# Kernel optimization log

Measured on AMD Instinct MI355X. Metric: run time of the kernel, lower is better.

Reference implementation:

```python
import jax, jax.numpy as jnp
import numpy as np

NUM_HEADS = 8

def setup_inputs() -> dict:
    key = jax.random.key(0)
    ks = jax.random.split(key, 7)
    B, N, K, C = 4, 16384, 16, 64
    pcd = jax.random.normal(ks[0], (B, C, N), dtype=jnp.float32)
    neighbors = jax.random.normal(ks[1], (B, C, N, K), dtype=jnp.float32)
    xyz = jax.random.normal(ks[2], (B, 3, N), dtype=jnp.float32)
    idx_all = jax.random.randint(ks[3], (B, N, K), 0, N)
    Wq = jax.random.normal(ks[4], (C, C + 3), dtype=jnp.float32) * 0.1
    Wk = jax.random.normal(ks[5], (C, C + 3), dtype=jnp.float32) * 0.1
    Wv = jax.random.normal(ks[6], (C, C + 3), dtype=jnp.float32) * 0.1
    return {"pcd": pcd, "neighbors": neighbors, "xyz": xyz,
            "Wq": Wq, "Wk": Wk, "Wv": Wv, "idx_all": idx_all}


def reference(pcd, neighbors, xyz, Wq, Wk, Wv, idx_all):
    B, C, N = pcd.shape
    K = neighbors.shape[-1]
    H = NUM_HEADS
    D = C // H
    # --- query: concat xyz, 1x1 conv, split heads ---
    pcd_cat = jnp.concatenate([pcd, xyz], axis=1)                 # (B, C+3, N)
    q = jnp.einsum('oc,bcn->bon', Wq, pcd_cat)                    # (B, C, N)
    q = q.reshape(B, H, D, N).transpose(0, 1, 3, 2)               # (B, H, N, D)
    # --- index_points: gather xyz at KNN indices (irregular gather) ---
    xyz_t = xyz.transpose(0, 2, 1)                                # (B, N, 3)
    rel_xyz = jax.vmap(lambda pts, ix: pts[ix])(xyz_t, idx_all)   # (B, N, K, 3)
    nb = jnp.concatenate([neighbors, rel_xyz.transpose(0, 3, 1, 2)], axis=1)  # (B, C+3, N, K)
    # --- key/value: 1x1 conv + split heads ---
    k = jnp.einsum('oc,bcnk->bonk', Wk, nb).reshape(B, H, D, N, K).transpose(0, 1, 3, 4, 2)  # (B,H,N,K,D)
    v = jnp.einsum('oc,bcnk->bonk', Wv, nb).reshape(B, H, D, N, K).transpose(0, 1, 3, 4, 2)  # (B,H,N,K,D)
    # --- local scalar-dot attention over the K neighbors of each point ---
    energy = jnp.einsum('bhnd,bhnkd->bhnk', q, k) / jnp.sqrt(jnp.float32(D))  # (B,H,N,K)
    attn = jax.nn.softmax(energy, axis=-1)
    x = jnp.einsum('bhnk,bhnkd->bhnd', attn, v)                   # (B, H, N, D)
    # (B,H,N,D) -> (B,N,H*D) -> (B, C, N), matching torch reshape/permute order
    out = x.transpose(0, 2, 1, 3).reshape(B, N, H * D).transpose(0, 2, 1)
    return out
```

## Files before the change

kernel.cpp:

```cpp
#include <hip/hip_runtime.h>
#include <math.h>

#define B_ 4
#define C_ 64
#define N_ 16384
#define K_ 16
#define H_ 8
#define CP 67
#define CPAD 68
#define NP 16
#define QSTRIDE 65
#define ESTRIDE 552

__device__ __align__(16) float wpad[3 * C_ * CPAD];

__global__ void setup_weights(const float* __restrict__ Wq,
                              const float* __restrict__ Wk,
                              const float* __restrict__ Wv) {
  int i = blockIdx.x * blockDim.x + threadIdx.x;
  if (i >= C_ * CPAD) return;
  int o = i / CPAD, j = i - o * CPAD;
  float q = 0.f, kk = 0.f, v = 0.f;
  if (j < CP) {
    q = Wq[o * CP + j] * 0.35355339059327373f;
    kk = Wk[o * CP + j];
    v = Wv[o * CP + j];
  }
  wpad[i] = q;
  wpad[C_ * CPAD + i] = kk;
  wpad[2 * C_ * CPAD + i] = v;
}

#define SWZ(v, imm) __int_as_float(__builtin_amdgcn_ds_swizzle(__float_as_int(v), (imm)))
#define XOR1 0x041F
#define XOR2 0x081F
#define XOR4 0x101F
#define XOR8 0x201F

__launch_bounds__(256, 3)
__global__ void pt_attn(const float* __restrict__ pcd,
                        const float* __restrict__ neighbors,
                        const float* __restrict__ xyz,
                        const int* __restrict__ idx_all,
                        float* __restrict__ out) {
  __shared__ __align__(16) float x_lds[NP * CPAD];
  __shared__ float q_lds[NP * QSTRIDE];
  __shared__ __align__(16) float e_lds[NP * ESTRIDE];

  const int tid = threadIdx.x;
  const int p = tid >> 4;
  const int k = tid & 15;
  const int blk = blockIdx.x;
  const int b = blk >> 10;
  const int n0 = (blk & 1023) << 4;
  const int n = n0 + p;

  float nb[CPAD];
  {
    const float* gp = neighbors + (size_t)b * (C_ * N_ * K_) + n0 * K_ + tid;
#pragma unroll
    for (int c = 0; c < C_; ++c)
      nb[c] = gp[(size_t)c * (N_ * K_)];
  }
  {
    const int idx = idx_all[(b * N_ + n) * K_ + k];
    const float* gx = xyz + (size_t)b * (3 * N_) + idx;
    nb[64] = gx[0];
    nb[65] = gx[N_];
    nb[66] = gx[2 * N_];
    nb[67] = 0.f;
  }

  {
    const int pp = tid & 15;
    const int c0 = tid >> 4;
#pragma unroll
    for (int it = 0; it < 4; ++it) {
      int c = c0 + it * 16;
      x_lds[pp * CPAD + c] = pcd[((size_t)b * C_ + c) * N_ + n0 + pp];
    }
    if (tid < 48)
      x_lds[pp * CPAD + 64 + c0] = xyz[((size_t)b * 3 + c0) * N_ + n0 + pp];
    if (tid < 16)
      x_lds[pp * CPAD + 67] = 0.f;
  }
  __syncthreads();

  {
    const float4* xr = (const float4*)(x_lds + p * CPAD);
    const float4* wq = (const float4*)(wpad) + 4 * k * 17;
    float a0 = 0.f, a1 = 0.f, a2 = 0.f, a3 = 0.f;
#pragma unroll
    for (int j4 = 0; j4 < 17; ++j4) {
      float4 xv = xr[j4];
      float4 w0 = wq[j4];
      float4 w1 = wq[17 + j4];
      float4 w2 = wq[34 + j4];
      float4 w3 = wq[51 + j4];
      a0 += w0.x * xv.x + w0.y * xv.y + w0.z * xv.z + w0.w * xv.w;
      a1 += w1.x * xv.x + w1.y * xv.y + w1.z * xv.z + w1.w * xv.w;
      a2 += w2.x * xv.x + w2.y * xv.y + w2.z * xv.z + w2.w * xv.w;
      a3 += w3.x * xv.x + w3.y * xv.y + w3.z * xv.z + w3.w * xv.w;
    }
    q_lds[p * QSTRIDE + 4 * k + 0] = a0;
    q_lds[p * QSTRIDE + 4 * k + 1] = a1;
    q_lds[p * QSTRIDE + 4 * k + 2] = a2;
    q_lds[p * QSTRIDE + 4 * k + 3] = a3;
  }
  __syncthreads();

  {
    const int h = k & 7;
    const int jh = k >> 3;
    float qa[8];
#pragma unroll
    for (int d = 0; d < 8; ++d)
      qa[d] = q_lds[p * QSTRIDE + h * 8 + d];
    const float4* wk = (const float4*)(wpad + C_ * CPAD) + h * 8 * 17;
    float4* er = (float4*)(e_lds + p * ESTRIDE + h * CPAD);
#pragma unroll
    for (int u = 0; u < 9; ++u) {
      int j4 = jh * 8 + u;
      float4 a = make_float4(0.f, 0.f, 0.f, 0.f);
#pragma unroll
      for (int d = 0; d < 8; ++d) {
        float4 w = wk[d * 17 + j4];
        a.x += qa[d] * w.x;
        a.y += qa[d] * w.y;
        a.z += qa[d] * w.z;
        a.w += qa[d] * w.w;
      }
      er[j4] = a;
    }
  }
  __syncthreads();

  float en[8];
#pragma unroll
  for (int h = 0; h < 8; ++h) en[h] = 0.f;
  {
    const float4* ep = (const float4*)(e_lds + p * ESTRIDE);
#pragma unroll
    for (int j4 = 0; j4 < 17; ++j4) {
#pragma unroll
      for (int h = 0; h < 8; ++h) {
        float4 e4 = ep[h * 17 + j4];
        en[h] += e4.x * nb[4 * j4 + 0] + e4.y * nb[4 * j4 + 1] +
                 e4.z * nb[4 * j4 + 2] + e4.w * nb[4 * j4 + 3];
      }
    }
  }
  float at[8];
#pragma unroll
  for (int h = 0; h < 8; ++h) {
    float m = en[h];
    m = fmaxf(m, SWZ(m, XOR1));
    m = fmaxf(m, SWZ(m, XOR2));
    m = fmaxf(m, SWZ(m, XOR4));
    m = fmaxf(m, SWZ(m, XOR8));
    float e = __expf(en[h] - m);
    float s = e;
    s += SWZ(s, XOR1);
    s += SWZ(s, XOR2);
    s += SWZ(s, XOR4);
    s += SWZ(s, XOR8);
    at[h] = e * __builtin_amdgcn_rcpf(s);
  }

  float ap[8];
  {
    const bool g2 = (k & 8) != 0;
    const bool g1 = (k & 4) != 0;
    const bool g0 = (k & 2) != 0;
    float t0[8], t1[8];
#pragma unroll
    for (int i = 0; i < 8; ++i) t0[i] = g2 ? at[i ^ 4] : at[i];
#pragma unroll
    for (int i = 0; i < 8; ++i) t1[i] = g1 ? t0[i ^ 2] : t0[i];
#pragma unroll
    for (int i = 0; i < 8; ++i) ap[i] = g0 ? t1[i ^ 1] : t1[i];
  }

  float xo0 = 0.f, xo1 = 0.f, xo2 = 0.f, xo3 = 0.f;
  const float4* wv = (const float4*)(wpad + 2 * C_ * CPAD) + 4 * k * 17;
#pragma unroll
  for (int j4 = 0; j4 < 17; ++j4) {
    float agg0, agg1, agg2, agg3;
#pragma unroll
    for (int u = 0; u < 4; ++u) {
      float nbj = nb[4 * j4 + u];
      float s0 = ap[0] * nbj, s1 = ap[1] * nbj, s2 = ap[2] * nbj, s3 = ap[3] * nbj;
      float s4 = ap[4] * nbj, s5 = ap[5] * nbj, s6 = ap[6] * nbj, s7 = ap[7] * nbj;
      s0 += SWZ(s4, XOR8);
      s1 += SWZ(s5, XOR8);
      s2 += SWZ(s6, XOR8);
      s3 += SWZ(s7, XOR8);
      s0 += SWZ(s2, XOR4);
      s1 += SWZ(s3, XOR4);
      s0 += SWZ(s1, XOR2);
      s0 += SWZ(s0, XOR1);
      if (u == 0) agg0 = s0;
      else if (u == 1) agg1 = s0;
      else if (u == 2) agg2 = s0;
      else agg3 = s0;
    }
    float4 w0 = wv[j4];
    float4 w1 = wv[17 + j4];
    float4 w2 = wv[34 + j4];
    float4 w3 = wv[51 + j4];
    xo0 += w0.x * agg0 + w0.y * agg1 + w0.z * agg2 + w0.w * agg3;
    xo1 += w1.x * agg0 + w1.y * agg1 + w1.z * agg2 + w1.w * agg3;
    xo2 += w2.x * agg0 + w2.y * agg1 + w2.z * agg2 + w2.w * agg3;
    xo3 += w3.x * agg0 + w3.y * agg1 + w3.z * agg2 + w3.w * agg3;
  }

  float* op = out + ((size_t)b * C_ + 4 * k) * N_ + n0 + p;
  op[0] = xo0;
  op[(size_t)N_] = xo1;
  op[2 * (size_t)N_] = xo2;
  op[3 * (size_t)N_] = xo3;
}

extern "C" void kernel_launch(void* const* d_in, const int* in_sizes, int n_in,
                              void* d_out, int out_size, void* d_ws, size_t ws_size,
                              hipStream_t stream) {
  const float* pcd = (const float*)d_in[0];
  const float* neighbors = (const float*)d_in[1];
  const float* xyz = (const float*)d_in[2];
  const float* Wq = (const float*)d_in[3];
  const float* Wk = (const float*)d_in[4];
  const float* Wv = (const float*)d_in[5];
  const int* idx = (const int*)d_in[6];
  float* out = (float*)d_out;

  setup_weights<<<(C_ * CPAD + 255) / 256, 256, 0, stream>>>(Wq, Wk, Wv);
  pt_attn<<<B_ * (N_ / NP), 256, 0, stream>>>(pcd, neighbors, xyz, idx, out);
}
```

Measured before the change: 630.1 us.

## Transpose weight layout, share q via DPP, drop q LDS round-trip, coalesce output

Stores the padded weights input-major so that consecutive lanes read contiguous output channels. The q projection is redistributed across lanes with DPP row rotations instead of passing through an LDS buffer and a barrier. Most ds_swizzle reductions become DPP ops, and one __syncthreads is replaced by an explicit lgkmcnt wait, which relies on each point's e_lds row being written and read within a single wavefront. Outputs are staged through LDS so they can be written as coalesced float4 stores, and launch bounds are raised to 4 blocks per CU, which risks register spills given the large per-thread nb array.

```diff
diff --git a/kernel.cpp b/kernel.cpp
--- a/kernel.cpp
+++ b/kernel.cpp
@@ -9,17 +9,17 @@
 #define CP 67
 #define CPAD 68
 #define NP 16
-#define QSTRIDE 65
 #define ESTRIDE 552
-
-__device__ __align__(16) float wpad[3 * C_ * CPAD];
+#define WSZ (C_ * CPAD)
+
+__device__ __align__(16) float wpad[3 * WSZ];
 
 __global__ void setup_weights(const float* __restrict__ Wq,
                               const float* __restrict__ Wk,
                               const float* __restrict__ Wv) {
   int i = blockIdx.x * blockDim.x + threadIdx.x;
-  if (i >= C_ * CPAD) return;
-  int o = i / CPAD, j = i - o * CPAD;
+  if (i >= WSZ) return;
+  int j = i >> 6, o = i & 63;
   float q = 0.f, kk = 0.f, v = 0.f;
   if (j < CP) {
     q = Wq[o * CP + j] * 0.35355339059327373f;
@@ -27,24 +27,30 @@
     v = Wv[o * CP + j];
   }
   wpad[i] = q;
-  wpad[C_ * CPAD + i] = kk;
-  wpad[2 * C_ * CPAD + i] = v;
+  wpad[WSZ + i] = kk;
+  wpad[2 * WSZ + i] = v;
 }
 
 #define SWZ(v, imm) __int_as_float(__builtin_amdgcn_ds_swizzle(__float_as_int(v), (imm)))
-#define XOR1 0x041F
-#define XOR2 0x081F
 #define XOR4 0x101F
-#define XOR8 0x201F
-
-__launch_bounds__(256, 3)
+
+#define DPP_XOR1 0xB1
+#define DPP_XOR2 0x4E
+#define DPP_ROR4 0x124
+#define DPP_ROR8 0x128
+template <int CTRL>
+__device__ __forceinline__ float dppf(float x) {
+  int i = __float_as_int(x);
+  return __int_as_float(__builtin_amdgcn_update_dpp(i, i, CTRL, 0xF, 0xF, false));
+}
+
+__launch_bounds__(256, 4)
 __global__ void pt_attn(const float* __restrict__ pcd,
                         const float* __restrict__ neighbors,
                         const float* __restrict__ xyz,
                         const int* __restrict__ idx_all,
                         float* __restrict__ out) {
   __shared__ __align__(16) float x_lds[NP * CPAD];
-  __shared__ float q_lds[NP * QSTRIDE];
   __shared__ __align__(16) float e_lds[NP * ESTRIDE];
 
   const int tid = threadIdx.x;
@@ -86,139 +92,152 @@
   }
   __syncthreads();
 
+  const int h = k & 7;
+  float a0 = 0.f, a1 = 0.f, a2 = 0.f, a3 = 0.f;
   {
     const float4* xr = (const float4*)(x_lds + p * CPAD);
-    const float4* wq = (const float4*)(wpad) + 4 * k * 17;
-    float a0 = 0.f, a1 = 0.f, a2 = 0.f, a3 = 0.f;
+    const float* wq = wpad + 8 * h + 4 * (k >> 3);
 #pragma unroll
     for (int j4 = 0; j4 < 17; ++j4) {
       float4 xv = xr[j4];
-      float4 w0 = wq[j4];
-      float4 w1 = wq[17 + j4];
-      float4 w2 = wq[34 + j4];
-      float4 w3 = wq[51 + j4];
-      a0 += w0.x * xv.x + w0.y * xv.y + w0.z * xv.z + w0.w * xv.w;
-      a1 += w1.x * xv.x + w1.y * xv.y + w1.z * xv.z + w1.w * xv.w;
-      a2 += w2.x * xv.x + w2.y * xv.y + w2.z * xv.z + w2.w * xv.w;
-      a3 += w3.x * xv.x + w3.y * xv.y + w3.z * xv.z + w3.w * xv.w;
-    }
-    q_lds[p * QSTRIDE + 4 * k + 0] = a0;
-    q_lds[p * QSTRIDE + 4 * k + 1] = a1;
-    q_lds[p * QSTRIDE + 4 * k + 2] = a2;
-    q_lds[p * QSTRIDE + 4 * k + 3] = a3;
-  }
+      float4 w0 = *(const float4*)(wq + (4 * j4 + 0) * 64);
+      float4 w1 = *(const float4*)(wq + (4 * j4 + 1) * 64);
+      float4 w2 = *(const float4*)(wq + (4 * j4 + 2) * 64);
+      float4 w3 = *(const float4*)(wq + (4 * j4 + 3) * 64);
+      a0 += w0.x * xv.x + w1.x * xv.y + w2.x * xv.z + w3.x * xv.w;
+      a1 += w0.y * xv.x + w1.y * xv.y + w2.y * xv.z + w3.y * xv.w;
+      a2 += w0.z * xv.x + w1.z * xv.y + w2.z * xv.z + w3.z * xv.w;
+      a3 += w0.w * xv.x + w1.w * xv.y + w2.w * xv.z + w3.w * xv.w;
+    }
+  }
+
+  {
+    float b0 = dppf<DPP_ROR8>(a0);
+    float b1 = dppf<DPP_ROR8>(a1);
+    float b2 = dppf<DPP_ROR8>(a2);
+    float b3 = dppf<DPP_ROR8>(a3);
+    const bool hi = (k & 8) != 0;
+    float qa0 = hi ? b0 : a0, qa1 = hi ? b1 : a1;
+    float qa2 = hi ? b2 : a2, qa3 = hi ? b3 : a3;
+    float qa4 = hi ? a0 : b0, qa5 = hi ? a1 : b1;
+    float qa6 = hi ? a2 : b2, qa7 = hi ? a3 : b3;
+
+    const float* wk = wpad + WSZ + 8 * h;
+    float4* er = (float4*)(e_lds + p * ESTRIDE + h * CPAD);
+    const int jb = (k >> 3) * 8;
+#pragma unroll
+    for (int u = 0; u < 9; ++u) {
+      int j4 = jb + u;
+      float r[4];
+#pragma unroll
+      for (int jj = 0; jj < 4; ++jj) {
+        const float4 wlo = *(const float4*)(wk + (4 * j4 + jj) * 64);
+        const float4 whi = *(const float4*)(wk + (4 * j4 + jj) * 64 + 4);
+        r[jj] = qa0 * wlo.x + qa1 * wlo.y + qa2 * wlo.z + qa3 * wlo.w +
+                qa4 * whi.x + qa5 * whi.y + qa6 * whi.z + qa7 * whi.w;
+      }
+      er[j4] = make_float4(r[0], r[1], r[2], r[3]);
+    }
+  }
+  asm volatile("s_waitcnt lgkmcnt(0)" ::: "memory");
+  __builtin_amdgcn_sched_barrier(0);
+
+  float en[8];
+#pragma unroll
+  for (int hh = 0; hh < 8; ++hh) en[hh] = 0.f;
+  {
+    const float4* ep = (const float4*)(e_lds + p * ESTRIDE);
+#pragma unroll
+    for (int j4 = 0; j4 < 17; ++j4) {
+#pragma unroll
+      for (int hh = 0; hh < 8; ++hh) {
+        float4 e4 = ep[hh * 17 + j4];
+        en[hh] += e4.x * nb[4 * j4 + 0] + e4.y * nb[4 * j4 + 1] +
+                  e4.z * nb[4 * j4 + 2] + e4.w * nb[4 * j4 + 3];
+      }
+    }
+  }
+  float at[8];
+#pragma unroll
+  for (int hh = 0; hh < 8; ++hh) {
+    float m = en[hh];
+    m = fmaxf(m, dppf<DPP_XOR1>(m));
+    m = fmaxf(m, dppf<DPP_XOR2>(m));
+    m = fmaxf(m, dppf<DPP_ROR4>(m));
+    m = fmaxf(m, dppf<DPP_ROR8>(m));
+    float e = __expf(en[hh] - m);
+    float s = e;
+    s += dppf<DPP_XOR1>(s);
+    s += dppf<DPP_XOR2>(s);
+    s += dppf<DPP_ROR4>(s);
+    s += dppf<DPP_ROR8>(s);
+    at[hh] = e * __builtin_amdgcn_rcpf(s);
+  }
+
+  const int g = (((k >> 3) & 1) << 2) | (((k >> 1) & 1) << 1) | (k & 1);
+  float ap[8];
+  {
+    float t0[8], t1[8];
+#pragma unroll
+    for (int i = 0; i < 8; ++i) t0[i] = (k & 8) ? at[i ^ 4] : at[i];
+#pragma unroll
+    for (int i = 0; i < 8; ++i) t1[i] = (k & 2) ? t0[i ^ 2] : t0[i];
+#pragma unroll
+    for (int i = 0; i < 8; ++i) ap[i] = (k & 1) ? t1[i ^ 1] : t1[i];
+  }
+
+  const int ob = 8 * g + (k & 4);
+  float xo0 = 0.f, xo1 = 0.f, xo2 = 0.f, xo3 = 0.f;
+  {
+    const float* wv = wpad + 2 * WSZ + ob;
+#pragma unroll
+    for (int j4 = 0; j4 < 17; ++j4) {
+      float agg0, agg1, agg2, agg3;
+#pragma unroll
+      for (int u = 0; u < 4; ++u) {
+        float nbj = nb[4 * j4 + u];
+        float s0 = ap[0] * nbj, s1 = ap[1] * nbj, s2 = ap[2] * nbj, s3 = ap[3] * nbj;
+        float s4 = ap[4] * nbj, s5 = ap[5] * nbj, s6 = ap[6] * nbj, s7 = ap[7] * nbj;
+        s0 += dppf<DPP_ROR8>(s4);
+        s1 += dppf<DPP_ROR8>(s5);
+        s2 += dppf<DPP_ROR8>(s6);
+        s3 += dppf<DPP_ROR8>(s7);
+        s0 += dppf<DPP_XOR2>(s2);
+        s1 += dppf<DPP_XOR2>(s3);
+        s0 += dppf<DPP_XOR1>(s1);
+        s0 += SWZ(s0, XOR4);
+        if (u == 0) agg0 = s0;
+        else if (u == 1) agg1 = s0;
+        else if (u == 2) agg2 = s0;
+        else agg3 = s0;
+      }
+      float4 w0 = *(const float4*)(wv + (4 * j4 + 0) * 64);
+      float4 w1 = *(const float4*)(wv + (4 * j4 + 1) * 64);
+      float4 w2 = *(const float4*)(wv + (4 * j4 + 2) * 64);
+      float4 w3 = *(const float4*)(wv + (4 * j4 + 3) * 64);
+      xo0 += w0.x * agg0 + w1.x * agg1 + w2.x * agg2 + w3.x * agg3;
+      xo1 += w0.y * agg0 + w1.y * agg1 + w2.y * agg2 + w3.y * agg3;
+      xo2 += w0.z * agg0 + w1.z * agg1 + w2.z * agg2 + w3.z * agg3;
+      xo3 += w0.w * agg0 + w1.w * agg1 + w2.w * agg2 + w3.w * agg3;
+    }
+  }
+
   __syncthreads();
-
-  {
-    const int h = k & 7;
-    const int jh = k >> 3;
-    float qa[8];
-#pragma unroll
-    for (int d = 0; d < 8; ++d)
-      qa[d] = q_lds[p * QSTRIDE + h * 8 + d];
-    const float4* wk = (const float4*)(wpad + C_ * CPAD) + h * 8 * 17;
-    float4* er = (float4*)(e_lds + p * ESTRIDE + h * CPAD);
-#pragma unroll
-    for (int u = 0; u < 9; ++u) {
-      int j4 = jh * 8 + u;
-      float4 a = make_float4(0.f, 0.f, 0.f, 0.f);
-#pragma unroll
-      for (int d = 0; d < 8; ++d) {
-        float4 w = wk[d * 17 + j4];
-        a.x += qa[d] * w.x;
-        a.y += qa[d] * w.y;
-        a.z += qa[d] * w.z;
-        a.w += qa[d] * w.w;
-      }
-      er[j4] = a;
-    }
+  {
+    float* ol = x_lds;
+    ol[(ob + 0) * 17 + p] = xo0;
+    ol[(ob + 1) * 17 + p] = xo1;
+    ol[(ob + 2) * 17 + p] = xo2;
+    ol[(ob + 3) * 17 + p] = xo3;
   }
   __syncthreads();
-
-  float en[8];
-#pragma unroll
-  for (int h = 0; h < 8; ++h) en[h] = 0.f;
-  {
-    const float4* ep = (const float4*)(e_lds + p * ESTRIDE);
-#pragma unroll
-    for (int j4 = 0; j4 < 17; ++j4) {
-#pragma unroll
-      for (int h = 0; h < 8; ++h) {
-        float4 e4 = ep[h * 17 + j4];
-        en[h] += e4.x * nb[4 * j4 + 0] + e4.y * nb[4 * j4 + 1] +
-                 e4.z * nb[4 * j4 + 2] + e4.w * nb[4 * j4 + 3];
-      }
-    }
-  }
-  float at[8];
-#pragma unroll
-  for (int h = 0; h < 8; ++h) {
-    float m = en[h];
-    m = fmaxf(m, SWZ(m, XOR1));
-    m = fmaxf(m, SWZ(m, XOR2));
-    m = fmaxf(m, SWZ(m, XOR4));
-    m = fmaxf(m, SWZ(m, XOR8));
-    float e = __expf(en[h] - m);
-    float s = e;
-    s += SWZ(s, XOR1);
-    s += SWZ(s, XOR2);
-    s += SWZ(s, XOR4);
-    s += SWZ(s, XOR8);
-    at[h] = e * __builtin_amdgcn_rcpf(s);
-  }
-
-  float ap[8];
-  {
-    const bool g2 = (k & 8) != 0;
-    const bool g1 = (k & 4) != 0;
-    const bool g0 = (k & 2) != 0;
-    float t0[8], t1[8];
-#pragma unroll
-    for (int i = 0; i < 8; ++i) t0[i] = g2 ? at[i ^ 4] : at[i];
-#pragma unroll
-    for (int i = 0; i < 8; ++i) t1[i] = g1 ? t0[i ^ 2] : t0[i];
-#pragma unroll
-    for (int i = 0; i < 8; ++i) ap[i] = g0 ? t1[i ^ 1] : t1[i];
-  }
-
-  float xo0 = 0.f, xo1 = 0.f, xo2 = 0.f, xo3 = 0.f;
-  const float4* wv = (const float4*)(wpad + 2 * C_ * CPAD) + 4 * k * 17;
-#pragma unroll
-  for (int j4 = 0; j4 < 17; ++j4) {
-    float agg0, agg1, agg2, agg3;
-#pragma unroll
-    for (int u = 0; u < 4; ++u) {
-      float nbj = nb[4 * j4 + u];
-      float s0 = ap[0] * nbj, s1 = ap[1] * nbj, s2 = ap[2] * nbj, s3 = ap[3] * nbj;
-      float s4 = ap[4] * nbj, s5 = ap[5] * nbj, s6 = ap[6] * nbj, s7 = ap[7] * nbj;
-      s0 += SWZ(s4, XOR8);
-      s1 += SWZ(s5, XOR8);
-      s2 += SWZ(s6, XOR8);
-      s3 += SWZ(s7, XOR8);
-      s0 += SWZ(s2, XOR4);
-      s1 += SWZ(s3, XOR4);
-      s0 += SWZ(s1, XOR2);
-      s0 += SWZ(s0, XOR1);
-      if (u == 0) agg0 = s0;
-      else if (u == 1) agg1 = s0;
-      else if (u == 2) agg2 = s0;
-      else agg3 = s0;
-    }
-    float4 w0 = wv[j4];
-    float4 w1 = wv[17 + j4];
-    float4 w2 = wv[34 + j4];
-    float4 w3 = wv[51 + j4];
-    xo0 += w0.x * agg0 + w0.y * agg1 + w0.z * agg2 + w0.w * agg3;
-    xo1 += w1.x * agg0 + w1.y * agg1 + w1.z * agg2 + w1.w * agg3;
-    xo2 += w2.x * agg0 + w2.y * agg1 + w2.z * agg2 + w2.w * agg3;
-    xo3 += w3.x * agg0 + w3.y * agg1 + w3.z * agg2 + w3.w * agg3;
-  }
-
-  float* op = out + ((size_t)b * C_ + 4 * k) * N_ + n0 + p;
-  op[0] = xo0;
-  op[(size_t)N_] = xo1;
-  op[2 * (size_t)N_] = xo2;
-  op[3 * (size_t)N_] = xo3;
+  {
+    const int o = tid >> 2;
+    const int pc = (tid & 3) << 2;
+    const float* ol = x_lds + o * 17 + pc;
+    float4 vo = make_float4(ol[0], ol[1], ol[2], ol[3]);
+    *(float4*)(out + ((size_t)b * C_ + o) * N_ + n0 + pc) = vo;
+  }
 }
 
 extern "C" void kernel_launch(void* const* d_in, const int* in_sizes, int n_in,
@@ -233,6 +252,6 @@
   const int* idx = (const int*)d_in[6];
   float* out = (float*)d_out;
 
-  setup_weights<<<(C_ * CPAD + 255) / 256, 256, 0, stream>>>(Wq, Wk, Wv);
+  setup_weights<<<(WSZ + 255) / 256, 256, 0, stream>>>(Wq, Wk, Wv);
   pt_attn<<<B_ * (N_ / NP), 256, 0, stream>>>(pcd, neighbors, xyz, idx, out);
 }
```

After: 680.5 us. 8.0% more time.
